# Kernel tuning notes

Measured on AMD Instinct MI355X. Metric: run time of the kernel, lower is better.

## Reference

```python
import jax, jax.numpy as jnp
import numpy as np

DIM = 512          # input_dimension (per-axis sinusoid width)
OUT_DIM = 256      # output_dimension


def _embed(z, c):
    # z: (N,) float positions -> (N, c) = [sin(z/1000^(i/c)) for odd i | cos(z/1000^(j/c)) for even j]
    i = jnp.arange(1, c, 2, dtype=jnp.float32)
    j = jnp.arange(0, c, 2, dtype=jnp.float32)
    s = jnp.sin(z[:, None] / (1000.0 ** (i / c)))
    co = jnp.cos(z[:, None] / (1000.0 ** (j / c)))
    return jnp.concatenate([s, co], axis=-1)


def setup_inputs() -> dict:
    key = jax.random.key(0)
    W_im = jax.random.normal(key, (OUT_DIM, 2 * DIM), dtype=jnp.float32)
    return {"W_im": W_im, "batch": 8, "channels": 512, "height": 64, "width": 64}


def reference(W_im, batch, channels, height, width):
    # Vectorized replacement of the triple nested loop: per-pixel vector is
    # cat(embed(x), embed(y)) of length 2*DIM; identical for every batch element.
    x = jnp.arange(height, dtype=jnp.float32)
    y = jnp.arange(width, dtype=jnp.float32)
    ex = _embed(x, DIM)  # (H, DIM)
    ey = _embed(y, DIM)  # (W, DIM)
    pos = jnp.concatenate(
        [jnp.broadcast_to(ex[:, None, :], (height, width, DIM)),
         jnp.broadcast_to(ey[None, :, :], (height, width, DIM))],
        axis=-1)  # (H, W, 2*DIM)
    out = jnp.einsum('od,hwd->hwo', W_im, pos)  # (H, W, OUT_DIM)
    # torch forward returns a list of B identical (H, W, OUT_DIM, 1) tensors; stack them.
    return jnp.broadcast_to(out[None], (batch, height, width, OUT_DIM))[..., None]
```

## Files before the change

kernel.cpp:

```cpp
#include <hip/hip_runtime.h>
#include <hip/hip_bf16.h>


#define DIMC 512
#define ODIM 256
#define NPOS 64

__global__ __launch_bounds__(256)
void pos_gemm_kernel(const float* __restrict__ Wim,
                     float* __restrict__ A, float* __restrict__ B) {
    __shared__ float e[DIMC];
    const int h = blockIdx.x;
    const int t = threadIdx.x;
    const float z = (float)h;
    const float ln1000 = 6.907755278982137f;

    float fs = __expf(-((float)(2 * t + 1) * (1.0f / 512.0f)) * ln1000);
    float fc = __expf(-((float)(2 * t)     * (1.0f / 512.0f)) * ln1000);
    e[t]       = sinf(z * fs);
    e[t + 256] = cosf(z * fc);
    __syncthreads();

    const float* wrow = Wim + (size_t)t * (2 * DIMC);
    float accA = 0.0f, accB = 0.0f;
#pragma unroll 4
    for (int d = 0; d < DIMC; d += 8) {
        float4 wa0 = *(const float4*)(wrow + d);
        float4 wa1 = *(const float4*)(wrow + d + 4);
        float4 wb0 = *(const float4*)(wrow + DIMC + d);
        float4 wb1 = *(const float4*)(wrow + DIMC + d + 4);
        float4 e0  = *(const float4*)(e + d);
        float4 e1  = *(const float4*)(e + d + 4);
        accA += wa0.x * e0.x + wa0.y * e0.y + wa0.z * e0.z + wa0.w * e0.w;
        accA += wa1.x * e1.x + wa1.y * e1.y + wa1.z * e1.z + wa1.w * e1.w;
        accB += wb0.x * e0.x + wb0.y * e0.y + wb0.z * e0.z + wb0.w * e0.w;
        accB += wb1.x * e1.x + wb1.y * e1.y + wb1.z * e1.z + wb1.w * e1.w;
    }
    A[h * ODIM + t] = accA;
    B[h * ODIM + t] = accB;
}

__global__ __launch_bounds__(256)
void pos_bcast_kernel(const float* __restrict__ A, const float* __restrict__ B,
                      float* __restrict__ out) {
    const int t = blockIdx.x * 256 + threadIdx.x;
    const int o4 = (t & 63) << 2;
    const int w  = (t >> 6) & 63;
    const int h  = (t >> 12) & 63;

    float4 a = *(const float4*)(A + h * ODIM + o4);
    float4 b = *(const float4*)(B + w * ODIM + o4);
    float4 r;
    r.x = a.x + b.x;
    r.y = a.y + b.y;
    r.z = a.z + b.z;
    r.w = a.w + b.w;
    *(float4*)(out + (size_t)t * 4) = r;
}

extern "C" void kernel_launch(void* const* d_in, const int* in_sizes, int n_in,
                              void* d_out, int out_size, void* d_ws, size_t ws_size,
                              hipStream_t stream) {
    const float* Wim = (const float*)d_in[0];
    float* A = (float*)d_ws;
    float* B = A + NPOS * ODIM;
    float* out = (float*)d_out;

    pos_gemm_kernel<<<NPOS, 256, 0, stream>>>(Wim, A, B);
    pos_bcast_kernel<<<8192, 256, 0, stream>>>(A, B, out);
}
```

Baseline: 106.2 us.

## Split GEMM reduction over K into four partial blocks and write batch copies per thread

The small projection GEMM now splits its reduction dimension into four chunks, giving 256 blocks instead of 64, so more compute units are busy. The partial sums are stored separately and combined in the broadcast kernel. The broadcast kernel now computes each (h,w,o) value once and writes it to all 8 batch slices, using 1024 blocks instead of 8192. This adds extra partial-sum reads in the broadcast step, and each thread issues eight strided stores.

```diff
diff --git a/kernel.cpp b/kernel.cpp
--- a/kernel.cpp
+++ b/kernel.cpp
@@ -2,70 +2,94 @@
 #include <hip/hip_bf16.h>
 
 
-#define DIMC 512
 #define ODIM 256
 #define NPOS 64
+#define KQ   128
 
 __global__ __launch_bounds__(256)
 void pos_gemm_kernel(const float* __restrict__ Wim,
-                     float* __restrict__ A, float* __restrict__ B) {
-    __shared__ float e[DIMC];
-    const int h = blockIdx.x;
+                     float* __restrict__ Apart, float* __restrict__ Bpart) {
+    __shared__ float e[KQ];
+    const int h = blockIdx.x >> 2;
+    const int q = blockIdx.x & 3;
     const int t = threadIdx.x;
-    const float z = (float)h;
-    const float ln1000 = 6.907755278982137f;
+    const int kbase = q * KQ;
 
-    float fs = __expf(-((float)(2 * t + 1) * (1.0f / 512.0f)) * ln1000);
-    float fc = __expf(-((float)(2 * t)     * (1.0f / 512.0f)) * ln1000);
-    e[t]       = sinf(z * fs);
-    e[t + 256] = cosf(z * fc);
+    if (t < KQ) {
+        const float ln1000 = 6.907755278982137f;
+        const float z = (float)h;
+        const int k = kbase + t;
+        float v;
+        if (k < 256) {
+            float f = __expf(-((float)(2 * k + 1) * (1.0f / 512.0f)) * ln1000);
+            v = sinf(z * f);
+        } else {
+            int j = k - 256;
+            float f = __expf(-((float)(2 * j) * (1.0f / 512.0f)) * ln1000);
+            v = cosf(z * f);
+        }
+        e[t] = v;
+    }
     __syncthreads();
 
-    const float* wrow = Wim + (size_t)t * (2 * DIMC);
+    const float* wA = Wim + (size_t)t * 1024 + kbase;
+    const float* wB = wA + 512;
     float accA = 0.0f, accB = 0.0f;
 #pragma unroll 4
-    for (int d = 0; d < DIMC; d += 8) {
-        float4 wa0 = *(const float4*)(wrow + d);
-        float4 wa1 = *(const float4*)(wrow + d + 4);
-        float4 wb0 = *(const float4*)(wrow + DIMC + d);
-        float4 wb1 = *(const float4*)(wrow + DIMC + d + 4);
-        float4 e0  = *(const float4*)(e + d);
-        float4 e1  = *(const float4*)(e + d + 4);
-        accA += wa0.x * e0.x + wa0.y * e0.y + wa0.z * e0.z + wa0.w * e0.w;
-        accA += wa1.x * e1.x + wa1.y * e1.y + wa1.z * e1.z + wa1.w * e1.w;
-        accB += wb0.x * e0.x + wb0.y * e0.y + wb0.z * e0.z + wb0.w * e0.w;
-        accB += wb1.x * e1.x + wb1.y * e1.y + wb1.z * e1.z + wb1.w * e1.w;
+    for (int d = 0; d < KQ; d += 8) {
+        float4 a0 = *(const float4*)(wA + d);
+        float4 a1 = *(const float4*)(wA + d + 4);
+        float4 b0 = *(const float4*)(wB + d);
+        float4 b1 = *(const float4*)(wB + d + 4);
+        float4 e0 = *(const float4*)(e + d);
+        float4 e1 = *(const float4*)(e + d + 4);
+        accA += a0.x * e0.x + a0.y * e0.y + a0.z * e0.z + a0.w * e0.w;
+        accA += a1.x * e1.x + a1.y * e1.y + a1.z * e1.z + a1.w * e1.w;
+        accB += b0.x * e0.x + b0.y * e0.y + b0.z * e0.z + b0.w * e0.w;
+        accB += b1.x * e1.x + b1.y * e1.y + b1.z * e1.z + b1.w * e1.w;
     }
-    A[h * ODIM + t] = accA;
-    B[h * ODIM + t] = accB;
+    Apart[q * (NPOS * ODIM) + h * ODIM + t] = accA;
+    Bpart[q * (NPOS * ODIM) + h * ODIM + t] = accB;
 }
 
 __global__ __launch_bounds__(256)
-void pos_bcast_kernel(const float* __restrict__ A, const float* __restrict__ B,
+void pos_bcast_kernel(const float* __restrict__ Apart,
+                      const float* __restrict__ Bpart,
                       float* __restrict__ out) {
-    const int t = blockIdx.x * 256 + threadIdx.x;
+    const int h  = blockIdx.x >> 4;
+    const int wt = blockIdx.x & 15;
+    const int t  = threadIdx.x;
     const int o4 = (t & 63) << 2;
-    const int w  = (t >> 6) & 63;
-    const int h  = (t >> 12) & 63;
+    const int w  = wt * 4 + (t >> 6);
 
-    float4 a = *(const float4*)(A + h * ODIM + o4);
-    float4 b = *(const float4*)(B + w * ODIM + o4);
-    float4 r;
-    r.x = a.x + b.x;
-    r.y = a.y + b.y;
-    r.z = a.z + b.z;
-    r.w = a.w + b.w;
-    *(float4*)(out + (size_t)t * 4) = r;
+    const int ai = h * ODIM + o4;
+    const int bi = w * ODIM + o4;
+    float4 r = make_float4(0.f, 0.f, 0.f, 0.f);
+#pragma unroll
+    for (int q = 0; q < 4; ++q) {
+        float4 a = *(const float4*)(Apart + q * (NPOS * ODIM) + ai);
+        float4 b = *(const float4*)(Bpart + q * (NPOS * ODIM) + bi);
+        r.x += a.x + b.x;
+        r.y += a.y + b.y;
+        r.z += a.z + b.z;
+        r.w += a.w + b.w;
+    }
+
+    const int base = (h << 14) | (w << 8) | o4;
+#pragma unroll
+    for (int b = 0; b < 8; ++b) {
+        *(float4*)(out + (size_t)((b << 20) | base)) = r;
+    }
 }
 
 extern "C" void kernel_launch(void* const* d_in, const int* in_sizes, int n_in,
                               void* d_out, int out_size, void* d_ws, size_t ws_size,
                               hipStream_t stream) {
     const float* Wim = (const float*)d_in[0];
-    float* A = (float*)d_ws;
-    float* B = A + NPOS * ODIM;
+    float* Apart = (float*)d_ws;
+    float* Bpart = Apart + 4 * NPOS * ODIM;
     float* out = (float*)d_out;
 
-    pos_gemm_kernel<<<NPOS, 256, 0, stream>>>(Wim, A, B);
-    pos_bcast_kernel<<<8192, 256, 0, stream>>>(A, B, out);
+    pos_gemm_kernel<<<NPOS * 4, 256, 0, stream>>>(Wim, Apart, Bpart);
+    pos_bcast_kernel<<<NPOS * 16, 256, 0, stream>>>(Apart, Bpart, out);
 }
```

After: 85.25 us. 1.25x faster.
